# Performance work log

Measured on AMD Instinct MI355X. Metric: run time of the kernel, lower is better.

Reference implementation:

```python
import jax, jax.numpy as jnp
import numpy as np

B, N, C = 4, 4096, 128
IK, CK = 9, 9  # inner_k, cross_k
BN_EPS = 1e-5


def setup_inputs() -> dict:
    key = jax.random.key(0)
    ks = jax.random.split(key, 8)
    d = {}
    d["x"] = jax.random.normal(ks[0], (B, N, C), jnp.float32)
    d["y"] = jax.random.normal(ks[1], (B, N, C), jnp.float32)
    d["x_mask"] = jnp.ones((B, N), jnp.float32)
    d["y_mask"] = jnp.ones((B, N), jnp.float32)
    specs = [("mr0", C, 2 * C), ("mr1", C, 2 * C), ("fc", C, C), ("f1", 4 * C, C), ("f2", C, 4 * C)]
    for (name, o, i), k in zip(specs, jax.random.split(ks[2], len(specs))):
        d[name + "_W"] = jax.random.normal(k, (o, i), jnp.float32) * 0.05
        d[name + "_b"] = jnp.zeros((o,), jnp.float32)
        d[name + "_g"] = jnp.ones((o,), jnp.float32)
        d[name + "_beta"] = jnp.zeros((o,), jnp.float32)
        d[name + "_m"] = jnp.zeros((o,), jnp.float32)
        d[name + "_v"] = jnp.ones((o,), jnp.float32)
    return d


def _sqdist(a, b):
    # a: [B,Na,C], b: [B,Nb,C] -> [B,Na,Nb]
    return (jnp.sum(a * a, -1)[:, :, None] + jnp.sum(b * b, -1)[:, None, :]
            - 2.0 * jnp.einsum('bnc,bmc->bnm', a, b))


def _knn(x, y):
    # neighbor indices into concat([x;y]) for every node: [B, Nx+Ny, IK+CK]
    Nx = x.shape[1]
    i_xx = jax.lax.top_k(-_sqdist(x, x), IK)[1]
    i_xy = jax.lax.top_k(-_sqdist(x, y), CK)[1] + Nx
    i_yy = jax.lax.top_k(-_sqdist(y, y), IK)[1] + Nx
    i_yx = jax.lax.top_k(-_sqdist(y, x), CK)[1]
    return jnp.concatenate([jnp.concatenate([i_xx, i_xy], -1),
                            jnp.concatenate([i_yy, i_yx], -1)], axis=1)


def _bn(h, g, b, m, v):
    # eval-mode BatchNorm over channel (last) axis
    return (h - m) * jax.lax.rsqrt(v + BN_EPS) * g + b


def _gelu(h):
    return jax.nn.gelu(h, approximate=False)


def _mrconv(f, nbr, W, b, g, be, m, v):
    # f: [B,Nt,C], nbr: [B,Nt,K] -> Conv(2C->C)+BN+GELU of interleaved [x, max_j(x_j-x_i)]
    xj = jax.vmap(lambda fb, nb: fb[nb])(f, nbr)          # [B,Nt,K,C] gather
    msg = jnp.max(xj - f[:, :, None, :], axis=2)          # [B,Nt,C]
    Bh, Nt, Ch = f.shape
    h = jnp.stack([f, msg], axis=-1).reshape(Bh, Nt, 2 * Ch)  # channel interleave as in torch reshape
    h = jnp.einsum('bnc,oc->bno', h, W) + b
    return _gelu(_bn(h, g, be, m, v))


def _forward(x, x_mask, y, y_mask,
             mr0_W, mr0_b, mr0_g, mr0_beta, mr0_m, mr0_v,
             mr1_W, mr1_b, mr1_g, mr1_beta, mr1_m, mr1_v,
             fc_W, fc_b, fc_g, fc_beta, fc_m, fc_v,
             f1_W, f1_b, f1_g, f1_beta, f1_m, f1_v,
             f2_W, f2_b, f2_g, f2_beta, f2_m, f2_v):
    Nx = x.shape[1]
    nbr = _knn(x, y)
    xy = jnp.concatenate([x, y], axis=1)
    xy = _mrconv(xy, nbr, mr0_W, mr0_b, mr0_g, mr0_beta, mr0_m, mr0_v) + xy
    xy = _mrconv(xy, nbr, mr1_W, mr1_b, mr1_g, mr1_beta, mr1_m, mr1_v) + xy
    xg, yg = xy[:, :Nx], xy[:, Nx:]

    def fc(h):
        return _bn(jnp.einsum('bnc,oc->bno', h, fc_W) + fc_b, fc_g, fc_beta, fc_m, fc_v)

    xo = fc(xg) + x
    yo = fc(yg) + y

    def ffn(h):
        r = h
        h = _gelu(_bn(jnp.einsum('bnc,oc->bno', h, f1_W) + f1_b, f1_g, f1_beta, f1_m, f1_v))
        h = _gelu(_bn(jnp.einsum('bnc,oc->bno', h, f2_W) + f2_b, f2_g, f2_beta, f2_m, f2_v))
        return h + r

    xo = ffn(xo) * x_mask[:, :, None]
    yo = ffn(yo) * y_mask[:, :, None]
    return xo, yo


def reference(x, x_mask, y, y_mask,
              mr0_W, mr0_b, mr0_g, mr0_beta, mr0_m, mr0_v,
              mr1_W, mr1_b, mr1_g, mr1_beta, mr1_m, mr1_v,
              fc_W, fc_b, fc_g, fc_beta, fc_m, fc_v,
              f1_W, f1_b, f1_g, f1_beta, f1_m, f1_v,
              f2_W, f2_b, f2_g, f2_beta, f2_m, f2_v):
    return _forward(x, x_mask, y, y_mask,
                    mr0_W, mr0_b, mr0_g, mr0_beta, mr0_m, mr0_v,
                    mr1_W, mr1_b, mr1_g, mr1_beta, mr1_m, mr1_v,
                    fc_W, fc_b, fc_g, fc_beta, fc_m, fc_v,
                    f1_W, f1_b, f1_g, f1_beta, f1_m, f1_v,
                    f2_W, f2_b, f2_g, f2_beta, f2_m, f2_v)
```

## Files before the change

### kernel.cpp

```cpp
#include <hip/hip_runtime.h>
#include <hip/hip_bf16.h>
#include <float.h>
#include <math.h>

#define BB 4
#define N1 4096
#define NT 8192
#define CH 128
#define NBRS 18
#define ZSEL 2.35f
#define LCAP 24
#define EQ 1024.0f
#define GQGAP 4
#define GQCOV 2

typedef __attribute__((ext_vector_type(8))) short s16x8;
typedef __attribute__((ext_vector_type(16))) float f32x16;

__device__ inline unsigned short f2bf(float v) {
  unsigned u = __float_as_uint(v);
  unsigned r = (u + 0x7FFFu + ((u >> 16) & 1u)) >> 16;
  return (unsigned short)r;
}

__device__ inline unsigned mapf(float f) {
  unsigned u = __float_as_uint(f);
  return (u & 0x80000000u) ? ~u : (u | 0x80000000u);
}

__global__ __launch_bounds__(256) void transpose_k(const float* __restrict__ in,
                                                   float* __restrict__ out,
                                                   int rows, int cols) {
  int t = blockIdx.x * 256 + threadIdx.x;
  if (t < rows * cols) {
    int r = t / cols, c = t % cols;
    out[c * rows + r] = in[t];
  }
}

__global__ __launch_bounds__(256) void norms_concat_k(const float* __restrict__ x,
                                                      const float* __restrict__ y,
                                                      float* __restrict__ xy,
                                                      float* __restrict__ norms) {
  int w = (blockIdx.x * 256 + threadIdx.x) >> 6;
  int lane = threadIdx.x & 63;
  int b = w >> 13, row = w & 8191;
  const float* src = (row < N1) ? (x + ((size_t)b * N1 + row) * CH)
                                : (y + ((size_t)b * N1 + (row - N1)) * CH);
  float2 v = *(const float2*)(src + lane * 2);
  *(float2*)(xy + (size_t)w * CH + lane * 2) = v;
  float s = v.x * v.x + v.y * v.y;
  for (int off = 32; off > 0; off >>= 1) s += __shfl_down(s, off);
  if (lane == 0) norms[w] = s;
}

__global__ __launch_bounds__(256) void cbt_k(const float* __restrict__ xy,
                                             unsigned short* __restrict__ cbt) {
  int t = blockIdx.x * 256 + threadIdx.x;
  int u = t >> 15, p = t & 32767;
  const float* src = xy + (size_t)p * CH + u * 8;
  unsigned hw[4], lw[4];
#pragma unroll
  for (int j = 0; j < 4; ++j) {
    float v0 = src[2 * j], v1 = src[2 * j + 1];
    unsigned short h0 = f2bf(v0), h1 = f2bf(v1);
    float r0 = v0 - __uint_as_float((unsigned)h0 << 16);
    float r1 = v1 - __uint_as_float((unsigned)h1 << 16);
    unsigned short l0 = f2bf(r0), l1 = f2bf(r1);
    hw[j] = (unsigned)h0 | ((unsigned)h1 << 16);
    lw[j] = (unsigned)l0 | ((unsigned)l1 << 16);
  }
  *(uint4*)&cbt[((size_t)u * 32768 + p) * 8] = make_uint4(hw[0], hw[1], hw[2], hw[3]);
  *(uint4*)&cbt[((size_t)(u + 16) * 32768 + p) * 8] = make_uint4(lw[0], lw[1], lw[2], lw[3]);
}

__global__ __launch_bounds__(256) void knn4_k(const unsigned short* __restrict__ cbt,
                                              const float* __restrict__ norms,
                                              int* __restrict__ nbr,
                                              int* __restrict__ cntg,
                                              unsigned* __restrict__ listA,
                                              unsigned* __restrict__ listB,
                                              unsigned short* __restrict__ fbl) {
  __shared__ unsigned short __align__(16) cst[2][32][32][8];
  __shared__ float cn_s[2][32];
  __shared__ unsigned lst[128][2][LCAP];
  __shared__ unsigned short lcnt[128][2];
  const int tid = threadIdx.x;
  const int qblk = blockIdx.x, z = blockIdx.y;
  const int b = z >> 2, combo = z & 3;
  const int qoff = (combo <= 1) ? 0 : N1;
  const int coff = (combo == 0 || combo == 3) ? 0 : N1;
  const int w = tid >> 6;
  const int cl = tid & 31;
  const int h = (tid >> 5) & 1;
  const int h4 = 4 * h;
  const int ql = w * 32 + cl;
  const int q = qblk * 128 + ql;
  const size_t qp = (size_t)b * NT + qoff + q;
  const size_t cb0 = (size_t)b * NT + coff;

  const s16x8* cv = (const s16x8*)cbt;
  s16x8 bh[8], bl[8];
#pragma unroll
  for (int s = 0; s < 8; ++s) {
    bh[s] = cv[(size_t)(2 * s + h) * 32768 + qp];
    bl[s] = cv[(size_t)(16 + 2 * s + h) * 32768 + qp];
  }

  const float nq = norms[qp];
  const float Tc = 128.f - ZSEL * sqrtf(256.f + 4.f * nq);
  int cnt = 0;

  const int su = tid >> 5, sc = tid & 31;
  const char* p0 = (const char*)&cbt[((size_t)(su) * 32768 + cb0 + sc) * 8];
  const char* p1 = (const char*)&cbt[((size_t)(8 + su) * 32768 + cb0 + sc) * 8];
  const char* p2 = (const char*)&cbt[((size_t)(16 + su) * 32768 + cb0 + sc) * 8];
  const char* p3 = (const char*)&cbt[((size_t)(24 + su) * 32768 + cb0 + sc) * 8];
  const float* pn = norms + cb0 + tid;

  uint4 st[4]; float cnreg = 0.f;
  st[0] = *(const uint4*)p0; p0 += 512;
  st[1] = *(const uint4*)p1; p1 += 512;
  st[2] = *(const uint4*)p2; p2 += 512;
  st[3] = *(const uint4*)p3; p3 += 512;
  if (tid < 32) { cnreg = *pn; pn += 32; }
  *(uint4*)&cst[0][su][sc][0] = st[0];
  *(uint4*)&cst[0][8 + su][sc][0] = st[1];
  *(uint4*)&cst[0][16 + su][sc][0] = st[2];
  *(uint4*)&cst[0][24 + su][sc][0] = st[3];
  if (tid < 32) cn_s[0][tid] = cnreg;
  __syncthreads();

  int buf = 0;
  for (int t = 0; t < 128; ++t) {
    if (t < 127) {
      st[0] = *(const uint4*)p0; p0 += 512;
      st[1] = *(const uint4*)p1; p1 += 512;
      st[2] = *(const uint4*)p2; p2 += 512;
      st[3] = *(const uint4*)p3; p3 += 512;
      if (tid < 32) { cnreg = *pn; pn += 32; }
    }
    f32x16 acc = {0.f,0.f,0.f,0.f,0.f,0.f,0.f,0.f,0.f,0.f,0.f,0.f,0.f,0.f,0.f,0.f};
#pragma unroll
    for (int s = 0; s < 8; ++s) {
      s16x8 a0 = *(const s16x8*)&cst[buf][2 * s + h][cl][0];
      s16x8 a1 = *(const s16x8*)&cst[buf][16 + 2 * s + h][cl][0];
      acc = __builtin_amdgcn_mfma_f32_32x32x16_bf16(a0, bh[s], acc, 0, 0, 0);
      acc = __builtin_amdgcn_mfma_f32_32x32x16_bf16(a0, bl[s], acc, 0, 0, 0);
      acc = __builtin_amdgcn_mfma_f32_32x32x16_bf16(a1, bh[s], acc, 0, 0, 0);
    }
    float4 c0 = *(const float4*)&cn_s[buf][h4];
    float4 c1 = *(const float4*)&cn_s[buf][8 + h4];
    float4 c2 = *(const float4*)&cn_s[buf][16 + h4];
    float4 c3 = *(const float4*)&cn_s[buf][24 + h4];
    const float cw[16] = {c0.x, c0.y, c0.z, c0.w, c1.x, c1.y, c1.z, c1.w,
                          c2.x, c2.y, c2.z, c2.w, c3.x, c3.y, c3.z, c3.w};
    const int ib = t * 32 + h4;
#pragma unroll
    for (int g = 0; g < 4; ++g) {
#pragma unroll
      for (int rr = 0; rr < 4; ++rr) {
        const int r = g * 4 + rr;
        float s = fmaf(-2.0f, acc[r], cw[r]);
        if (s <= Tc) {
          int e = (int)((Tc - s) * EQ);
          e = e > 65535 ? 65535 : e;
          unsigned key = ((unsigned)e << 16) | (unsigned)(4095 - (ib + g * 8 + rr));
          if (cnt < LCAP) lst[ql][h][cnt] = key;
          ++cnt;
        }
      }
    }
    if (t < 127) {
      *(uint4*)&cst[buf ^ 1][su][sc][0] = st[0];
      *(uint4*)&cst[buf ^ 1][8 + su][sc][0] = st[1];
      *(uint4*)&cst[buf ^ 1][16 + su][sc][0] = st[2];
      *(uint4*)&cst[buf ^ 1][24 + su][sc][0] = st[3];
      if (tid < 32) cn_s[buf ^ 1][tid] = cnreg;
    }
    __syncthreads();
    buf ^= 1;
  }
  lcnt[ql][h] = (unsigned short)cnt;
  __syncthreads();

  if (tid < 128) {
    const int mq = tid;
    const int gq = z * 4096 + qblk * 128 + mq;
    const int c0 = lcnt[mq][0], c1 = lcnt[mq][1];
    const bool over = (c0 > LCAP) || (c1 > LCAP);
    const int n0 = c0 > LCAP ? LCAP : c0;
    const int n1 = c1 > LCAP ? LCAP : c1;
    const int m = n0 + n1;
    unsigned top[10];
#pragma unroll
    for (int j = 0; j < 10; ++j) top[j] = 0u;
    for (int li = 0; li < 2; ++li) {
      const int n = li ? n1 : n0;
      for (int i = 0; i < n; ++i) {
        unsigned key = lst[mq][li][i];
        if (key > top[9]) {
#pragma unroll
          for (int j = 0; j < 10; ++j) {
            bool sw = key > top[j];
            unsigned tv = top[j];
            top[j] = sw ? key : tv;
            key = sw ? tv : key;
          }
        }
      }
    }
    const unsigned e8 = top[8] >> 16, e9 = top[9] >> 16;
    const bool cov = !over && (m >= 9) && (e8 >= GQCOV);
    const bool ok = cov && (m == 9 || (e8 - e9) >= GQGAP);
    const int qg = qblk * 128 + mq;
    const int row = (combo <= 1) ? qg : (N1 + qg);
    const int slot = (combo == 0 || combo == 2) ? 0 : 9;
    const int ioff = (combo == 1 || combo == 2) ? N1 : 0;
    int* dst = nbr + ((size_t)b * NT + row) * NBRS + slot;
    if (ok) {
#pragma unroll
      for (int s = 0; s < 9; ++s)
        dst[s] = (int)(4095u - (top[s] & 0xffffu)) + ioff;
    } else if (!cov) {
      int idx = atomicAdd(&cntg[1], 1);
      listB[idx] = (unsigned)gq;
    } else {
      int idx = atomicAdd(&cntg[0], 1);
      listA[idx] = ((unsigned)m << 16) | (unsigned)gq;
      unsigned short* fp = fbl + (size_t)gq * 48;
      int p = 0;
      for (int i = 0; i < n0; ++i) fp[p++] = (unsigned short)(4095u - (lst[mq][0][i] & 0xffffu));
      for (int i = 0; i < n1; ++i) fp[p++] = (unsigned short)(4095u - (lst[mq][1][i] & 0xffffu));
    }
  }
}

__global__ __launch_bounds__(256) void rerank_sl_k(const float* __restrict__ xy,
                                                   const float* __restrict__ norms,
                                                   const unsigned short* __restrict__ fbl,
                                                   const unsigned* __restrict__ listA,
                                                   const int* __restrict__ cntg,
                                                   int* __restrict__ nbr) {
  const int lane = threadIdx.x & 63;
  const int wv = threadIdx.x >> 6;
  const int nA = cntg[0];
  for (int i = blockIdx.x * 4 + wv; i < nA; i += gridDim.x * 4) {
    const unsigned ent = listA[i];
    const int gq = (int)(ent & 0xffffu);
    const int m = (int)(ent >> 16);
    const int z = gq >> 12, q = gq & 4095;
    const int b = z >> 2, combo = z & 3;
    const int qoff = (combo <= 1) ? 0 : N1;
    const int coff = (combo == 0 || combo == 3) ? 0 : N1;
    const size_t cq = (size_t)b * NT + coff;
    const int row = (combo <= 1) ? q : (N1 + q);
    const int slot = (combo == 0 || combo == 2) ? 0 : 9;
    const int ioff = (combo == 1 || combo == 2) ? N1 : 0;
    int* dst = nbr + ((size_t)b * NT + row) * NBRS + slot;
    const float* qrow = xy + ((size_t)b * NT + qoff + q) * CH;

    int ci = 0; float de = FLT_MAX;
    if (lane < m) {
      ci = (int)fbl[(size_t)gq * 48 + lane];
      const float* crow = xy + (cq + ci) * CH;
      const float cnv = norms[cq + ci];
      float a0 = 0.f, a1 = 0.f, a2 = 0.f, a3 = 0.f;
#pragma unroll
      for (int k = 0; k < 32; ++k) {
        float4 qv = *(const float4*)(qrow + k * 4);
        float4 cv2 = *(const float4*)(crow + k * 4);
        a0 = fmaf(qv.x, cv2.x, a0); a1 = fmaf(qv.y, cv2.y, a1);
        a2 = fmaf(qv.z, cv2.z, a2); a3 = fmaf(qv.w, cv2.w, a3);
      }
      de = cnv - 2.0f * ((a0 + a1) + (a2 + a3));
    }
    unsigned long long key = ((unsigned long long)mapf(de) << 32) | (unsigned)ci;
    if (lane >= m) key = ~0ull;
    int xr = 0;
#pragma unroll 1
    for (int k = 0; k < m; ++k) {
      unsigned long long kk = __shfl(key, k);
      xr += (kk < key) ? 1 : 0;
    }
    if (lane < m && xr < 9) dst[xr] = ci + ioff;
  }
}

__global__ __launch_bounds__(256) void rerank_fs_k(const float* __restrict__ xy,
                                                   const float* __restrict__ norms,
                                                   const unsigned* __restrict__ listB,
                                                   const int* __restrict__ cntg,
                                                   int* __restrict__ nbr) {
  __shared__ unsigned long long ms[4][576];
  __shared__ unsigned long long wk[36];
  const int tid = threadIdx.x;
  const int lane = tid & 63, wv = tid >> 6;
  const int nB = cntg[1];
  for (int i = blockIdx.x; i < nB; i += gridDim.x) {
    const int gq = (int)listB[i];
    const int z = gq >> 12, q = gq & 4095;
    const int b = z >> 2, combo = z & 3;
    const int qoff = (combo <= 1) ? 0 : N1;
    const int coff = (combo == 0 || combo == 3) ? 0 : N1;
    const size_t cq = (size_t)b * NT + coff;
    const int row = (combo <= 1) ? q : (N1 + q);
    const int slot = (combo == 0 || combo == 2) ? 0 : 9;
    const int ioff = (combo == 1 || combo == 2) ? N1 : 0;
    int* dst = nbr + ((size_t)b * NT + row) * NBRS + slot;
    const float* qrow = xy + ((size_t)b * NT + qoff + q) * CH;

    unsigned long long bl9[9];
#pragma unroll
    for (int j = 0; j < 9; ++j) bl9[j] = ~0ull;
    for (int it = 0; it < 16; ++it) {
      const int cc = (it * 4 + wv) * 64 + lane;
      const float* crow = xy + (cq + cc) * CH;
      float a0 = 0.f, a1 = 0.f, a2 = 0.f, a3 = 0.f;
#pragma unroll
      for (int k = 0; k < 32; ++k) {
        float4 qv = *(const float4*)(qrow + k * 4);
        float4 cv2 = *(const float4*)(crow + k * 4);
        a0 = fmaf(qv.x, cv2.x, a0); a1 = fmaf(qv.y, cv2.y, a1);
        a2 = fmaf(qv.z, cv2.z, a2); a3 = fmaf(qv.w, cv2.w, a3);
      }
      float d2v = norms[cq + cc] - 2.0f * ((a0 + a1) + (a2 + a3));
      unsigned long long key = ((unsigned long long)mapf(d2v) << 32) | (unsigned)cc;
      if (key < bl9[8]) {
#pragma unroll
        for (int jj = 0; jj < 9; ++jj) {
          bool sw = key < bl9[jj];
          unsigned long long tv = bl9[jj];
          bl9[jj] = sw ? key : tv;
          key = sw ? tv : key;
        }
      }
    }
#pragma unroll
    for (int s = 0; s < 9; ++s) ms[wv][lane * 9 + s] = bl9[s];
    int ptr = 0;
    for (int s = 0; s < 9; ++s) {
      unsigned long long hd = ms[wv][lane * 9 + ptr];
      unsigned long long mn = hd;
#pragma unroll
      for (int off = 1; off < 64; off <<= 1) {
        unsigned long long ot = __shfl_xor(mn, off);
        mn = (ot < mn) ? ot : mn;
      }
      unsigned long long wm = __ballot(hd == mn);
      int wl = __ffsll(wm) - 1;
      if (lane == wl) ptr++;
      if (lane == 0) wk[wv * 9 + s] = mn;
    }
    __syncthreads();
    if (wv == 0) {
      unsigned long long key = (lane < 36) ? wk[lane] : ~0ull;
      int xr = 0;
#pragma unroll 1
      for (int k = 0; k < 36; ++k) {
        unsigned long long kk = __shfl(key, k);
        xr += (kk < key) ? 1 : 0;
      }
      if (lane < 36 && xr < 9) dst[xr] = (int)(unsigned)(key & 0xffffffffull) + ioff;
    }
    __syncthreads();
  }
}

__global__ __launch_bounds__(256) void mrconv_k(const float* __restrict__ in,
                                                const int* __restrict__ nbr,
                                                const float* __restrict__ Wt,
                                                const float* __restrict__ bias,
                                                const float* __restrict__ gam,
                                                const float* __restrict__ bet,
                                                const float* __restrict__ mean,
                                                const float* __restrict__ var,
                                                float* __restrict__ out) {
  __shared__ float h[32][260];
  const int tid = threadIdx.x;
  const int pt0 = blockIdx.x * 32;
  {
    const int w = tid >> 6, lane = tid & 63;
    for (int pp = 0; pp < 8; ++pp) {
      const int p = w * 8 + pp;
      const int n = pt0 + p;
      const int b = n >> 13;
      const float* frow = in + (size_t)n * CH;
      float2 f2 = *(const float2*)(frow + lane * 2);
      float mx = -FLT_MAX, my = -FLT_MAX;
      const int* nb = nbr + (size_t)n * NBRS;
      for (int j = 0; j < NBRS; ++j) {
        int idx = nb[j];
        const float* vrow = in + ((size_t)b * NT + idx) * CH;
        float2 v2 = *(const float2*)(vrow + lane * 2);
        mx = fmaxf(mx, v2.x - f2.x);
        my = fmaxf(my, v2.y - f2.y);
      }
      h[p][lane * 4 + 0] = f2.x; h[p][lane * 4 + 1] = mx;
      h[p][lane * 4 + 2] = f2.y; h[p][lane * 4 + 3] = my;
    }
  }
  __syncthreads();
  const int o = tid & 127, gg = tid >> 7;
  float acc[16];
#pragma unroll
  for (int p = 0; p < 16; ++p) acc[p] = 0.f;
  for (int k = 0; k < 256; k += 4) {
    float w0 = Wt[(k + 0) * CH + o], w1 = Wt[(k + 1) * CH + o];
    float w2 = Wt[(k + 2) * CH + o], w3 = Wt[(k + 3) * CH + o];
#pragma unroll
    for (int p = 0; p < 16; ++p) {
      float4 hv = *(const float4*)&h[gg * 16 + p][k];
      acc[p] = fmaf(hv.x, w0, acc[p]);
      acc[p] = fmaf(hv.y, w1, acc[p]);
      acc[p] = fmaf(hv.z, w2, acc[p]);
      acc[p] = fmaf(hv.w, w3, acc[p]);
    }
  }
  const float sc = gam[o] / sqrtf(var[o] + 1e-5f);
  const float bs = bias[o], mo = mean[o], be = bet[o];
#pragma unroll
  for (int p = 0; p < 16; ++p) {
    const int n = pt0 + gg * 16 + p;
    float hv = acc[p] + bs;
    float bn = (hv - mo) * sc + be;
    float gl = 0.5f * bn * (1.0f + erff(bn * 0.70710678118654752f));
    out[(size_t)n * CH + o] = gl + h[gg * 16 + p][2 * o];
  }
}

__global__ __launch_bounds__(256) void fc_k(const float* __restrict__ in,
                                            const float* __restrict__ Wt,
                                            const float* __restrict__ bias,
                                            const float* __restrict__ gam,
                                            const float* __restrict__ bet,
                                            const float* __restrict__ mean,
                                            const float* __restrict__ var,
                                            const float* __restrict__ xres,
                                            const float* __restrict__ yres,
                                            float* __restrict__ out) {
  __shared__ float s[32][132];
  const int tid = threadIdx.x;
  const int pt0 = blockIdx.x * 32;
  {
    const int w = tid >> 6, lane = tid & 63;
    for (int pp = 0; pp < 8; ++pp) {
      const int p = w * 8 + pp, n = pt0 + p;
      float2 v = *(const float2*)(in + (size_t)n * CH + lane * 2);
      s[p][lane * 2] = v.x; s[p][lane * 2 + 1] = v.y;
    }
  }
  __syncthreads();
  const int o = tid & 127, gg = tid >> 7;
  float acc[16];
#pragma unroll
  for (int p = 0; p < 16; ++p) acc[p] = 0.f;
  for (int k = 0; k < 128; k += 4) {
    float w0 = Wt[(k + 0) * CH + o], w1 = Wt[(k + 1) * CH + o];
    float w2 = Wt[(k + 2) * CH + o], w3 = Wt[(k + 3) * CH + o];
#pragma unroll
    for (int p = 0; p < 16; ++p) {
      float4 hv = *(const float4*)&s[gg * 16 + p][k];
      acc[p] = fmaf(hv.x, w0, fmaf(hv.y, w1, fmaf(hv.z, w2, fmaf(hv.w, w3, acc[p]))));
    }
  }
  const float sc = gam[o] / sqrtf(var[o] + 1e-5f);
  const float bs = bias[o], mo = mean[o], be = bet[o];
#pragma unroll
  for (int p = 0; p < 16; ++p) {
    const int n = pt0 + gg * 16 + p;
    const int b = n >> 13, row = n & 8191;
    float bn = (acc[p] + bs - mo) * sc + be;
    float res = (row < N1) ? xres[((size_t)b * N1 + row) * CH + o]
                           : yres[((size_t)b * N1 + row - N1) * CH + o];
    out[(size_t)n * CH + o] = bn + res;
  }
}

__global__ __launch_bounds__(256) void ffn_k(const float* __restrict__ u,
                                             const float* __restrict__ W1t,
                                             const float* __restrict__ b1,
                                             const float* __restrict__ g1,
                                             const float* __restrict__ be1,
                                             const float* __restrict__ m1,
                                             const float* __restrict__ v1,
                                             const float* __restrict__ W2t,
                                             const float* __restrict__ b2,
                                             const float* __restrict__ g2,
                                             const float* __restrict__ be2,
                                             const float* __restrict__ m2,
                                             const float* __restrict__ v2,
                                             const float* __restrict__ xmask,
                                             const float* __restrict__ ymask,
                                             float* __restrict__ outbuf) {
  __shared__ float su[16][132];
  __shared__ float h1[16][516];
  const int tid = threadIdx.x;
  const int pt0 = blockIdx.x * 16;
  {
    const int w = tid >> 6, lane = tid & 63;
    for (int pp = 0; pp < 4; ++pp) {
      const int p = w * 4 + pp, n = pt0 + p;
      float2 v = *(const float2*)(u + (size_t)n * CH + lane * 2);
      su[p][lane * 2] = v.x; su[p][lane * 2 + 1] = v.y;
    }
  }
  __syncthreads();
  {
    const int o2 = tid;
    float a1[16], a2[16];
#pragma unroll
    for (int p = 0; p < 16; ++p) { a1[p] = 0.f; a2[p] = 0.f; }
    for (int k = 0; k < 128; k += 2) {
      float wA0 = W1t[(k + 0) * 512 + o2], wB0 = W1t[(k + 0) * 512 + o2 + 256];
      float wA1 = W1t[(k + 1) * 512 + o2], wB1 = W1t[(k + 1) * 512 + o2 + 256];
#pragma unroll
      for (int p = 0; p < 16; ++p) {
        float2 uv = *(const float2*)&su[p][k];
        a1[p] = fmaf(uv.x, wA0, fmaf(uv.y, wA1, a1[p]));
        a2[p] = fmaf(uv.x, wB0, fmaf(uv.y, wB1, a2[p]));
      }
    }
    float scA = g1[o2] / sqrtf(v1[o2] + 1e-5f);
    float scB = g1[o2 + 256] / sqrtf(v1[o2 + 256] + 1e-5f);
    float bsA = b1[o2], moA = m1[o2], beA = be1[o2];
    float bsB = b1[o2 + 256], moB = m1[o2 + 256], beB = be1[o2 + 256];
#pragma unroll
    for (int p = 0; p < 16; ++p) {
      float hA = (a1[p] + bsA - moA) * scA + beA;
      float hB = (a2[p] + bsB - moB) * scB + beB;
      h1[p][o2] = 0.5f * hA * (1.0f + erff(hA * 0.70710678118654752f));
      h1[p][o2 + 256] = 0.5f * hB * (1.0f + erff(hB * 0.70710678118654752f));
    }
  }
  __syncthreads();
  const int o = tid & 127, gg = tid >> 7;
  float acc[8];
#pragma unroll
  for (int p = 0; p < 8; ++p) acc[p] = 0.f;
  for (int k = 0; k < 512; k += 4) {
    float w0 = W2t[(k + 0) * CH + o], w1 = W2t[(k + 1) * CH + o];
    float w2 = W2t[(k + 2) * CH + o], w3 = W2t[(k + 3) * CH + o];
#pragma unroll
    for (int p = 0; p < 8; ++p) {
      float4 hv = *(const float4*)&h1[gg * 8 + p][k];
      acc[p] = fmaf(hv.x, w0, fmaf(hv.y, w1, fmaf(hv.z, w2, fmaf(hv.w, w3, acc[p]))));
    }
  }
  const float sc = g2[o] / sqrtf(v2[o] + 1e-5f);
  const float bs = b2[o], mo = m2[o], be = be2[o];
#pragma unroll
  for (int p = 0; p < 8; ++p) {
    const int n = pt0 + gg * 8 + p;
    const int b = n >> 13, row = n & 8191;
    float bn = (acc[p] + bs - mo) * sc + be;
    float gl = 0.5f * bn * (1.0f + erff(bn * 0.70710678118654752f));
    float res = su[gg * 8 + p][o];
    float msk; size_t oidx;
    if (row < N1) {
      msk = xmask[(size_t)b * N1 + row];
      oidx = ((size_t)b * N1 + row) * CH + o;
    } else {
      msk = ymask[(size_t)b * N1 + row - N1];
      oidx = (size_t)BB * N1 * CH + ((size_t)b * N1 + row - N1) * CH + o;
    }
    outbuf[oidx] = (gl + res) * msk;
  }
}

extern "C" void kernel_launch(void* const* d_in, const int* in_sizes, int n_in,
                              void* d_out, int out_size, void* d_ws, size_t ws_size,
                              hipStream_t stream) {
  const float* x  = (const float*)d_in[0];
  const float* y  = (const float*)d_in[1];
  const float* xm = (const float*)d_in[2];
  const float* ym = (const float*)d_in[3];
  const float* mr0W = (const float*)d_in[4];
  const float* mr1W = (const float*)d_in[10];
  const float* fcW  = (const float*)d_in[16];
  const float* f1W  = (const float*)d_in[22];
  const float* f2W  = (const float*)d_in[28];

  char* ws = (char*)d_ws;
  float*          xyA   = (float*)(ws + 0);
  unsigned short* cbt   = (unsigned short*)(ws + 16777216);
  float*          xyB   = (float*)(ws + 16777216);
  float*          norms = (float*)(ws + 33554432);
  int*            cntg  = (int*)(ws + 33685504);
  unsigned*       listA = (unsigned*)(ws + 33689600);
  unsigned*       listB = (unsigned*)(ws + 33951744);
  unsigned short* fbl   = (unsigned short*)(ws + 34213888);
  int*            nbr   = (int*)(ws + 40505344);
  float*          mr0t  = (float*)(ws + 42864640);
  float*          mr1t  = (float*)(ws + 42995712);
  float*          fct   = (float*)(ws + 43126784);
  float*          f1t   = (float*)(ws + 43192320);
  float*          f2t   = (float*)(ws + 43454464);

  hipMemsetAsync(cntg, 0, 8, stream);

  transpose_k<<<(128 * 256 + 255) / 256, 256, 0, stream>>>(mr0W, mr0t, 128, 256);
  transpose_k<<<(128 * 256 + 255) / 256, 256, 0, stream>>>(mr1W, mr1t, 128, 256);
  transpose_k<<<(128 * 128 + 255) / 256, 256, 0, stream>>>(fcW, fct, 128, 128);
  transpose_k<<<(512 * 128 + 255) / 256, 256, 0, stream>>>(f1W, f1t, 512, 128);
  transpose_k<<<(128 * 512 + 255) / 256, 256, 0, stream>>>(f2W, f2t, 128, 512);

  norms_concat_k<<<8192, 256, 0, stream>>>(x, y, xyA, norms);
  cbt_k<<<2048, 256, 0, stream>>>(xyA, cbt);
  knn4_k<<<dim3(32, 16), 256, 0, stream>>>(cbt, norms, nbr, cntg, listA, listB, fbl);
  rerank_sl_k<<<256, 256, 0, stream>>>(xyA, norms, fbl, listA, cntg, nbr);
  rerank_fs_k<<<256, 256, 0, stream>>>(xyA, norms, listB, cntg, nbr);

  mrconv_k<<<1024, 256, 0, stream>>>(xyA, nbr, mr0t,
      (const float*)d_in[5], (const float*)d_in[6], (const float*)d_in[7],
      (const float*)d_in[8], (const float*)d_in[9], xyB);
  mrconv_k<<<1024, 256, 0, stream>>>(xyB, nbr, mr1t,
      (const float*)d_in[11], (const float*)d_in[12], (const float*)d_in[13],
      (const float*)d_in[14], (const float*)d_in[15], xyA);

  fc_k<<<1024, 256, 0, stream>>>(xyA, fct,
      (const float*)d_in[17], (const float*)d_in[18], (const float*)d_in[19],
      (const float*)d_in[20], (const float*)d_in[21], x, y, xyB);

  ffn_k<<<2048, 256, 0, stream>>>(xyB,
      f1t, (const float*)d_in[23], (const float*)d_in[24], (const float*)d_in[25],
      (const float*)d_in[26], (const float*)d_in[27],
      f2t, (const float*)d_in[29], (const float*)d_in[30], (const float*)d_in[31],
      (const float*)d_in[32], (const float*)d_in[33],
      xm, ym, (float*)d_out);
}
```

Before: 667.9 us.

## Split KNN candidate scan across two grid halves with register top-8 and merge kernel

The KNN kernel now splits the candidate range into two halves along a new grid dimension, doubling the block count. Each thread keeps a register-resident sorted top-8 via insertion instead of appending to a capped shared-memory list. A new merge kernel combines the four partial lists per query, checks certainty, and routes queries to the rerank lists. This removes the shared list storage and the serial per-query merge tail inside the KNN kernel. It adds an extra launch and global traffic for the partial lists, and changes the key quantisation and certainty thresholds, which may route more queries to the slower fallback rerank.

```diff
diff --git a/kernel.cpp b/kernel.cpp
--- a/kernel.cpp
+++ b/kernel.cpp
@@ -9,10 +9,10 @@
 #define CH 128
 #define NBRS 18
 #define ZSEL 2.35f
-#define LCAP 24
-#define EQ 1024.0f
-#define GQGAP 4
-#define GQCOV 2
+#define EQ 4096.0f
+#define GQGAP 6
+#define GQCOV 4
+#define KPP 8
 
 typedef __attribute__((ext_vector_type(8))) short s16x8;
 typedef __attribute__((ext_vector_type(16))) float f32x16;
@@ -27,6 +27,18 @@
   unsigned u = __float_as_uint(f);
   return (u & 0x80000000u) ? ~u : (u | 0x80000000u);
 }
+
+#define INS8U(l, key0)                          \
+  {                                             \
+    unsigned nk = key0;                         \
+    _Pragma("unroll")                           \
+    for (int j = 0; j < KPP; ++j) {             \
+      bool sw = nk > l[j];                      \
+      unsigned tv = l[j];                       \
+      l[j] = sw ? nk : tv;                      \
+      nk = sw ? tv : nk;                        \
+    }                                           \
+  }
 
 __global__ __launch_bounds__(256) void transpose_k(const float* __restrict__ in,
                                                    float* __restrict__ out,
@@ -74,19 +86,14 @@
   *(uint4*)&cbt[((size_t)(u + 16) * 32768 + p) * 8] = make_uint4(lw[0], lw[1], lw[2], lw[3]);
 }
 
-__global__ __launch_bounds__(256) void knn4_k(const unsigned short* __restrict__ cbt,
+__global__ __launch_bounds__(256) void knn6_k(const unsigned short* __restrict__ cbt,
                                               const float* __restrict__ norms,
-                                              int* __restrict__ nbr,
-                                              int* __restrict__ cntg,
-                                              unsigned* __restrict__ listA,
-                                              unsigned* __restrict__ listB,
-                                              unsigned short* __restrict__ fbl) {
+                                              unsigned* __restrict__ pl,
+                                              unsigned char* __restrict__ cnts) {
   __shared__ unsigned short __align__(16) cst[2][32][32][8];
   __shared__ float cn_s[2][32];
-  __shared__ unsigned lst[128][2][LCAP];
-  __shared__ unsigned short lcnt[128][2];
   const int tid = threadIdx.x;
-  const int qblk = blockIdx.x, z = blockIdx.y;
+  const int qblk = blockIdx.x, half = blockIdx.y, z = blockIdx.z;
   const int b = z >> 2, combo = z & 3;
   const int qoff = (combo <= 1) ? 0 : N1;
   const int coff = (combo == 0 || combo == 3) ? 0 : N1;
@@ -97,7 +104,7 @@
   const int ql = w * 32 + cl;
   const int q = qblk * 128 + ql;
   const size_t qp = (size_t)b * NT + qoff + q;
-  const size_t cb0 = (size_t)b * NT + coff;
+  const size_t cb0 = (size_t)b * NT + coff + half * 2048;
 
   const s16x8* cv = (const s16x8*)cbt;
   s16x8 bh[8], bl[8];
@@ -110,6 +117,9 @@
   const float nq = norms[qp];
   const float Tc = 128.f - ZSEL * sqrtf(256.f + 4.f * nq);
   int cnt = 0;
+  unsigned lA[KPP];
+#pragma unroll
+  for (int j = 0; j < KPP; ++j) lA[j] = 0u;
 
   const int su = tid >> 5, sc = tid & 31;
   const char* p0 = (const char*)&cbt[((size_t)(su) * 32768 + cb0 + sc) * 8];
@@ -132,8 +142,8 @@
   __syncthreads();
 
   int buf = 0;
-  for (int t = 0; t < 128; ++t) {
-    if (t < 127) {
+  for (int t = 0; t < 64; ++t) {
+    if (t < 63) {
       st[0] = *(const uint4*)p0; p0 += 512;
       st[1] = *(const uint4*)p1; p1 += 512;
       st[2] = *(const uint4*)p2; p2 += 512;
@@ -155,23 +165,20 @@
     float4 c3 = *(const float4*)&cn_s[buf][24 + h4];
     const float cw[16] = {c0.x, c0.y, c0.z, c0.w, c1.x, c1.y, c1.z, c1.w,
                           c2.x, c2.y, c2.z, c2.w, c3.x, c3.y, c3.z, c3.w};
-    const int ib = t * 32 + h4;
-#pragma unroll
-    for (int g = 0; g < 4; ++g) {
-#pragma unroll
-      for (int rr = 0; rr < 4; ++rr) {
-        const int r = g * 4 + rr;
-        float s = fmaf(-2.0f, acc[r], cw[r]);
-        if (s <= Tc) {
-          int e = (int)((Tc - s) * EQ);
-          e = e > 65535 ? 65535 : e;
-          unsigned key = ((unsigned)e << 16) | (unsigned)(4095 - (ib + g * 8 + rr));
-          if (cnt < LCAP) lst[ql][h][cnt] = key;
-          ++cnt;
-        }
-      }
-    }
-    if (t < 127) {
+    const int ib = half * 2048 + t * 32 + h4;
+#pragma unroll
+    for (int r = 0; r < 16; ++r) {
+      const int idx = ib + (r & 3) + 8 * (r >> 2);
+      float s = fmaf(-2.0f, acc[r], cw[r]);
+      if (s <= Tc) {
+        ++cnt;
+        int e = (int)((Tc - s) * EQ);
+        e = e > 0xFFFFF ? 0xFFFFF : e;
+        unsigned key = ((unsigned)e << 12) | (unsigned)(4095 - idx);
+        if (key > lA[KPP - 1]) INS8U(lA, key);
+      }
+    }
+    if (t < 63) {
       *(uint4*)&cst[buf ^ 1][su][sc][0] = st[0];
       *(uint4*)&cst[buf ^ 1][8 + su][sc][0] = st[1];
       *(uint4*)&cst[buf ^ 1][16 + su][sc][0] = st[2];
@@ -181,64 +188,88 @@
     __syncthreads();
     buf ^= 1;
   }
-  lcnt[ql][h] = (unsigned short)cnt;
-  __syncthreads();
-
-  if (tid < 128) {
-    const int mq = tid;
-    const int gq = z * 4096 + qblk * 128 + mq;
-    const int c0 = lcnt[mq][0], c1 = lcnt[mq][1];
-    const bool over = (c0 > LCAP) || (c1 > LCAP);
-    const int n0 = c0 > LCAP ? LCAP : c0;
-    const int n1 = c1 > LCAP ? LCAP : c1;
-    const int m = n0 + n1;
-    unsigned top[10];
-#pragma unroll
-    for (int j = 0; j < 10; ++j) top[j] = 0u;
-    for (int li = 0; li < 2; ++li) {
-      const int n = li ? n1 : n0;
-      for (int i = 0; i < n; ++i) {
-        unsigned key = lst[mq][li][i];
-        if (key > top[9]) {
-#pragma unroll
-          for (int j = 0; j < 10; ++j) {
-            bool sw = key > top[j];
-            unsigned tv = top[j];
-            top[j] = sw ? key : tv;
-            key = sw ? tv : key;
-          }
-        }
-      }
-    }
-    const unsigned e8 = top[8] >> 16, e9 = top[9] >> 16;
-    const bool cov = !over && (m >= 9) && (e8 >= GQCOV);
-    const bool ok = cov && (m == 9 || (e8 - e9) >= GQGAP);
-    const int qg = qblk * 128 + mq;
-    const int row = (combo <= 1) ? qg : (N1 + qg);
-    const int slot = (combo == 0 || combo == 2) ? 0 : 9;
-    const int ioff = (combo == 1 || combo == 2) ? N1 : 0;
-    int* dst = nbr + ((size_t)b * NT + row) * NBRS + slot;
-    if (ok) {
-#pragma unroll
-      for (int s = 0; s < 9; ++s)
-        dst[s] = (int)(4095u - (top[s] & 0xffffu)) + ioff;
-    } else if (!cov) {
-      int idx = atomicAdd(&cntg[1], 1);
-      listB[idx] = (unsigned)gq;
-    } else {
-      int idx = atomicAdd(&cntg[0], 1);
-      listA[idx] = ((unsigned)m << 16) | (unsigned)gq;
-      unsigned short* fp = fbl + (size_t)gq * 48;
-      int p = 0;
-      for (int i = 0; i < n0; ++i) fp[p++] = (unsigned short)(4095u - (lst[mq][0][i] & 0xffffu));
-      for (int i = 0; i < n1; ++i) fp[p++] = (unsigned short)(4095u - (lst[mq][1][i] & 0xffffu));
-    }
+
+  const size_t lbase = (((size_t)(z * 4096 + q) * 2 + h) * 2 + half) * KPP;
+#pragma unroll
+  for (int j = 0; j < KPP; ++j) pl[lbase + j] = lA[j];
+  cnts[((size_t)(z * 4096 + q) * 2 + h) * 2 + half] =
+      (unsigned char)(cnt > 255 ? 255 : cnt);
+}
+
+__global__ __launch_bounds__(256) void merge_cert_k(const unsigned* __restrict__ pl,
+                                                    const unsigned char* __restrict__ cnts,
+                                                    int* __restrict__ nbr,
+                                                    int* __restrict__ cntg,
+                                                    unsigned* __restrict__ listA,
+                                                    unsigned* __restrict__ listB) {
+  const int gq = blockIdx.x * 256 + threadIdx.x;
+  const int z = gq >> 12, q = gq & 4095;
+  const int b = z >> 2, combo = z & 3;
+  const uchar4 cc = *(const uchar4*)&cnts[(size_t)gq * 4];
+  const int c[4] = {cc.x, cc.y, cc.z, cc.w};
+  int k[4];
+#pragma unroll
+  for (int i = 0; i < 4; ++i) k[i] = c[i] > KPP ? KPP : c[i];
+  const int m_true = c[0] + c[1] + c[2] + c[3];
+  const int m_kept = k[0] + k[1] + k[2] + k[3];
+
+  unsigned arr[32];
+  {
+    const uint4* pb = (const uint4*)&pl[(size_t)gq * 32];
+#pragma unroll
+    for (int i = 0; i < 8; ++i) {
+      uint4 v = pb[i];
+      arr[i * 4 + 0] = v.x; arr[i * 4 + 1] = v.y;
+      arr[i * 4 + 2] = v.z; arr[i * 4 + 3] = v.w;
+    }
+  }
+#pragma unroll
+  for (int i = 0; i < 4; ++i)
+#pragma unroll
+    for (int p = 0; p < KPP; ++p)
+      if (p >= k[i]) arr[i * KPP + p] = 0u;
+
+  unsigned mg[10];
+  unsigned cur = 0u; bool first = true;
+#pragma unroll
+  for (int s = 0; s < 10; ++s) {
+    unsigned mx = 0u;
+#pragma unroll
+    for (int j = 0; j < 32; ++j) {
+      unsigned v = arr[j];
+      v = (first || v < cur) ? v : 0u;
+      mx = v > mx ? v : mx;
+    }
+    mg[s] = mx; cur = mx; first = false;
+  }
+  const unsigned e8 = mg[8] >> 12, e9 = mg[9] >> 12;
+  bool incomplete = false;
+#pragma unroll
+  for (int i = 0; i < 4; ++i)
+    if (c[i] > KPP && arr[i * KPP + KPP - 1] >= mg[9]) incomplete = true;
+
+  const int row = (combo <= 1) ? q : (N1 + q);
+  const int slot = (combo == 0 || combo == 2) ? 0 : 9;
+  const int ioff = (combo == 1 || combo == 2) ? N1 : 0;
+  int* dst = nbr + ((size_t)b * NT + row) * NBRS + slot;
+
+  if (m_true < 9 || m_kept < 9 || incomplete || e8 < GQCOV) {
+    int idx = atomicAdd(&cntg[1], 1);
+    listB[idx] = (unsigned)gq;
+  } else if (m_true == 9 || (e8 - e9) >= GQGAP) {
+#pragma unroll
+    for (int s = 0; s < 9; ++s)
+      dst[s] = (int)(4095u - (mg[s] & 0xFFFu)) + ioff;
+  } else {
+    int idx = atomicAdd(&cntg[0], 1);
+    listA[idx] = ((unsigned)m_kept << 16) | (unsigned)gq;
   }
 }
 
 __global__ __launch_bounds__(256) void rerank_sl_k(const float* __restrict__ xy,
                                                    const float* __restrict__ norms,
-                                                   const unsigned short* __restrict__ fbl,
+                                                   const unsigned* __restrict__ pl,
+                                                   const unsigned char* __restrict__ cnts,
                                                    const unsigned* __restrict__ listA,
                                                    const int* __restrict__ cntg,
                                                    int* __restrict__ nbr) {
@@ -260,28 +291,36 @@
     int* dst = nbr + ((size_t)b * NT + row) * NBRS + slot;
     const float* qrow = xy + ((size_t)b * NT + qoff + q) * CH;
 
+    const uchar4 cc = *(const uchar4*)&cnts[(size_t)gq * 4];
+    const int k0 = cc.x > KPP ? KPP : cc.x, k1 = cc.y > KPP ? KPP : cc.y;
+    const int k2 = cc.z > KPP ? KPP : cc.z;
+    const int o1 = k0, o2 = k0 + k1, o3 = o2 + k2;
+
     int ci = 0; float de = FLT_MAX;
     if (lane < m) {
-      ci = (int)fbl[(size_t)gq * 48 + lane];
+      const int li = (lane >= o1) + (lane >= o2) + (lane >= o3);
+      const int pos = lane - (li == 0 ? 0 : li == 1 ? o1 : li == 2 ? o2 : o3);
+      const unsigned key = pl[(size_t)gq * 32 + li * KPP + pos];
+      ci = (int)(4095u - (key & 0xFFFu));
       const float* crow = xy + (cq + ci) * CH;
       const float cnv = norms[cq + ci];
       float a0 = 0.f, a1 = 0.f, a2 = 0.f, a3 = 0.f;
 #pragma unroll
-      for (int k = 0; k < 32; ++k) {
-        float4 qv = *(const float4*)(qrow + k * 4);
-        float4 cv2 = *(const float4*)(crow + k * 4);
+      for (int kk = 0; kk < 32; ++kk) {
+        float4 qv = *(const float4*)(qrow + kk * 4);
+        float4 cv2 = *(const float4*)(crow + kk * 4);
         a0 = fmaf(qv.x, cv2.x, a0); a1 = fmaf(qv.y, cv2.y, a1);
         a2 = fmaf(qv.z, cv2.z, a2); a3 = fmaf(qv.w, cv2.w, a3);
       }
       de = cnv - 2.0f * ((a0 + a1) + (a2 + a3));
     }
-    unsigned long long key = ((unsigned long long)mapf(de) << 32) | (unsigned)ci;
-    if (lane >= m) key = ~0ull;
+    unsigned long long key64 = ((unsigned long long)mapf(de) << 32) | (unsigned)ci;
+    if (lane >= m) key64 = ~0ull;
     int xr = 0;
 #pragma unroll 1
-    for (int k = 0; k < m; ++k) {
-      unsigned long long kk = __shfl(key, k);
-      xr += (kk < key) ? 1 : 0;
+    for (int kk = 0; kk < m; ++kk) {
+      unsigned long long kk2 = __shfl(key64, kk);
+      xr += (kk2 < key64) ? 1 : 0;
     }
     if (lane < m && xr < 9) dst[xr] = ci + ioff;
   }
@@ -318,9 +357,9 @@
       const float* crow = xy + (cq + cc) * CH;
       float a0 = 0.f, a1 = 0.f, a2 = 0.f, a3 = 0.f;
 #pragma unroll
-      for (int k = 0; k < 32; ++k) {
-        float4 qv = *(const float4*)(qrow + k * 4);
-        float4 cv2 = *(const float4*)(crow + k * 4);
+      for (int kk = 0; kk < 32; ++kk) {
+        float4 qv = *(const float4*)(qrow + kk * 4);
+        float4 cv2 = *(const float4*)(crow + kk * 4);
         a0 = fmaf(qv.x, cv2.x, a0); a1 = fmaf(qv.y, cv2.y, a1);
         a2 = fmaf(qv.z, cv2.z, a2); a3 = fmaf(qv.w, cv2.w, a3);
       }
@@ -357,9 +396,9 @@
       unsigned long long key = (lane < 36) ? wk[lane] : ~0ull;
       int xr = 0;
 #pragma unroll 1
-      for (int k = 0; k < 36; ++k) {
-        unsigned long long kk = __shfl(key, k);
-        xr += (kk < key) ? 1 : 0;
+      for (int kk = 0; kk < 36; ++kk) {
+        unsigned long long kk2 = __shfl(key, kk);
+        xr += (kk2 < key) ? 1 : 0;
       }
       if (lane < 36 && xr < 9) dst[xr] = (int)(unsigned)(key & 0xffffffffull) + ioff;
     }
@@ -589,13 +628,14 @@
   int*            cntg  = (int*)(ws + 33685504);
   unsigned*       listA = (unsigned*)(ws + 33689600);
   unsigned*       listB = (unsigned*)(ws + 33951744);
-  unsigned short* fbl   = (unsigned short*)(ws + 34213888);
-  int*            nbr   = (int*)(ws + 40505344);
-  float*          mr0t  = (float*)(ws + 42864640);
-  float*          mr1t  = (float*)(ws + 42995712);
-  float*          fct   = (float*)(ws + 43126784);
-  float*          f1t   = (float*)(ws + 43192320);
-  float*          f2t   = (float*)(ws + 43454464);
+  unsigned*       pl    = (unsigned*)(ws + 34213888);
+  unsigned char*  cnts  = (unsigned char*)(ws + 42602496);
+  int*            nbr   = (int*)(ws + 42864640);
+  float*          mr0t  = (float*)(ws + 45223936);
+  float*          mr1t  = (float*)(ws + 45355008);
+  float*          fct   = (float*)(ws + 45486080);
+  float*          f1t   = (float*)(ws + 45551616);
+  float*          f2t   = (float*)(ws + 45813760);
 
   hipMemsetAsync(cntg, 0, 8, stream);
 
@@ -607,8 +647,9 @@
 
   norms_concat_k<<<8192, 256, 0, stream>>>(x, y, xyA, norms);
   cbt_k<<<2048, 256, 0, stream>>>(xyA, cbt);
-  knn4_k<<<dim3(32, 16), 256, 0, stream>>>(cbt, norms, nbr, cntg, listA, listB, fbl);
-  rerank_sl_k<<<256, 256, 0, stream>>>(xyA, norms, fbl, listA, cntg, nbr);
+  knn6_k<<<dim3(32, 2, 16), 256, 0, stream>>>(cbt, norms, pl, cnts);
+  merge_cert_k<<<256, 256, 0, stream>>>(pl, cnts, nbr, cntg, listA, listB);
+  rerank_sl_k<<<256, 256, 0, stream>>>(xyA, norms, pl, cnts, listA, cntg, nbr);
   rerank_fs_k<<<256, 256, 0, stream>>>(xyA, norms, listB, cntg, nbr);
 
   mrconv_k<<<1024, 256, 0, stream>>>(xyA, nbr, mr0t,
```

Result: slower. 704.7 us (+5.5%).
